# Kernel tuning notes

Hardware: AMD Instinct MI355X
Metric: run time of the kernel (lower is better)

Reference implementation:

```python
import jax, jax.numpy as jnp
import numpy as np

EPS = 1e-8


def _mp_match(v1, v2, w):
    """Fused multi-perspective cosine match.
    v1, v2: (G, L, D); w: (P, D). Returns (G, L, P).
    cos_p(l) = <w_p*v1_l, w_p*v2_l> / max(||w_p*v1_l|| * ||w_p*v2_l||, eps)
    """
    w2 = w * w  # (P, D)
    num = jnp.einsum('gld,pd->glp', v1 * v2, w2)
    n1 = jnp.sqrt(jnp.einsum('gld,pd->glp', v1 * v1, w2))
    n2 = jnp.sqrt(jnp.einsum('gld,pd->glp', v2 * v2, w2))
    return num / jnp.maximum(n1 * n2, EPS)


def setup_inputs() -> dict:
    key = jax.random.key(0)
    k1, k2 = jax.random.split(key)
    n_graphs = 64
    nodes_per_graph = 2048
    dim = 128  # must equal perspectives (mp_w is square)
    N = n_graphs * nodes_per_graph
    feats = jax.random.normal(k1, (N, dim), dtype=jnp.float32)
    graph_idx = jnp.repeat(jnp.arange(n_graphs, dtype=jnp.int64), nodes_per_graph)
    mp_w = jax.random.uniform(k2, (dim, dim), dtype=jnp.float32)  # torch.rand
    return {"feats": feats, "mp_w": mp_w, "graph_idx": graph_idx, "n_graphs": n_graphs}


def reference(feats, mp_w, graph_idx, n_graphs):
    N, d = feats.shape
    L = N // n_graphs  # equal-size graphs, graph_idx is sorted/contiguous
    g = feats.reshape(n_graphs, L, d)
    p = g[0::2]  # (G/2, L, d) premise graphs
    h = g[1::2]  # (G/2, L, d) hypothesis graphs
    # cosine_attention is a plain dot product (no normalization in source)
    att = jnp.einsum('gld,gmd->glm', p, h)        # (G/2, Lp, Lh)
    att_p = jnp.einsum('glm,gmd->gld', att, h)     # (G/2, Lp, d)
    att_h = jnp.einsum('glm,gld->gmd', att, p)     # (G/2, Lh, d)
    multi_p = _mp_match(p, att_p, mp_w)            # (G/2, Lp, P)
    multi_h = _mp_match(h, att_h, mp_w)            # (G/2, Lh, P)
    # original concatenates [p0, h0, p1, h1, ...] along node axis
    P = mp_w.shape[0]
    out = jnp.stack([multi_p, multi_h], axis=1).reshape(n_graphs * L, P)
    return out
```

## Files before the change

### kernel.cpp

```cpp
#include <hip/hip_runtime.h>
#include <math.h>

#define D 128
#define GRAPHS 64

typedef __attribute__((ext_vector_type(8))) short bf16x8;
typedef __attribute__((ext_vector_type(4))) float f32x4;

__device__ __forceinline__ unsigned short f2bf(float f) {
  union { float f; unsigned u; } v; v.f = f;
  unsigned r = v.u + 0x7fffu + ((v.u >> 16) & 1u);
  return (unsigned short)(r >> 16);
}
__device__ __forceinline__ float bf2f(unsigned short h) {
  union { unsigned u; float f; } v; v.u = ((unsigned)h) << 16;
  return v.f;
}
__device__ __forceinline__ unsigned short truncbf(float f) {
  union { float f; unsigned u; } v; v.f = f;
  return (unsigned short)(v.u >> 16);
}

__global__ __launch_bounds__(256) void gram_mfma_kernel(
    const float* __restrict__ feats, float* __restrict__ partial,
    int L, int KS) {
  const int g = blockIdx.x / KS;
  const int s = blockIdx.x - g * KS;
  const int chunk = L / KS;
  const float* __restrict__ X = feats + ((size_t)g * L + (size_t)s * chunk) * D;

  __shared__ unsigned short sXT[128][40];
  const int tid = threadIdx.x;
  const int wv = tid >> 6, lane = tid & 63, quad = lane >> 4, ln = lane & 15;

  f32x4 acc[2][8];
#pragma unroll
  for (int rt = 0; rt < 2; ++rt)
#pragma unroll
    for (int ct = 0; ct < 8; ++ct) acc[rt][ct] = (f32x4)(0.f);

  for (int k0 = 0; k0 < chunk; k0 += 32) {
    __syncthreads();
#pragma unroll
    for (int v = 0; v < 2; ++v) {
      int idx = tid + v * 256;
      int k2 = idx & 15, d4 = idx >> 4;
      int k = k2 * 2, dd = d4 * 4;
      float4 r0 = *(const float4*)(X + (size_t)(k0 + k) * D + dd);
      float4 r1 = *(const float4*)(X + (size_t)(k0 + k + 1) * D + dd);
      const float* p0 = (const float*)&r0;
      const float* p1 = (const float*)&r1;
#pragma unroll
      for (int i = 0; i < 4; ++i) {
        unsigned pack = (unsigned)f2bf(p0[i]) | ((unsigned)f2bf(p1[i]) << 16);
        *(unsigned*)&sXT[dd + i][k] = pack;
      }
    }
    __syncthreads();
    bf16x8 af[2], bfr[8];
#pragma unroll
    for (int rt = 0; rt < 2; ++rt)
      af[rt] = *(const bf16x8*)&sXT[32 * wv + 16 * rt + ln][quad * 8];
#pragma unroll
    for (int ct = 0; ct < 8; ++ct)
      bfr[ct] = *(const bf16x8*)&sXT[16 * ct + ln][quad * 8];
#pragma unroll
    for (int rt = 0; rt < 2; ++rt)
#pragma unroll
      for (int ct = 0; ct < 8; ++ct)
        acc[rt][ct] = __builtin_amdgcn_mfma_f32_16x16x32_bf16(
            af[rt], bfr[ct], acc[rt][ct], 0, 0, 0);
  }

  float* P = partial + (size_t)blockIdx.x * (D * D);
#pragma unroll
  for (int rt = 0; rt < 2; ++rt)
#pragma unroll
    for (int ct = 0; ct < 8; ++ct)
#pragma unroll
      for (int r = 0; r < 4; ++r)
        P[(size_t)(32 * wv + 16 * rt + quad * 4 + r) * D + 16 * ct + ln] =
            acc[rt][ct][r];
}

__global__ __launch_bounds__(256) void gram_reduce_bf_kernel(
    const float* __restrict__ partial, unsigned short* __restrict__ gram,
    int KS) {
  int idx = blockIdx.x * 256 + threadIdx.x;
  int g = idx >> 14;
  const float* P = partial + (size_t)g * KS * (D * D) + (idx & (D * D - 1));
  float s = 0.f;
  for (int k = 0; k < KS; ++k) s += P[(size_t)k * (D * D)];
  gram[idx] = f2bf(s);
}

__global__ __launch_bounds__(256) void w2_kernel(
    const float* __restrict__ w, unsigned short* __restrict__ w2) {
  int idx = blockIdx.x * 256 + threadIdx.x;
  float v = w[idx];
  w2[idx] = f2bf(v * v);
}

__global__ __launch_bounds__(256) void fused_mfma_kernel(
    const float* __restrict__ feats, const unsigned short* __restrict__ gram,
    const unsigned short* __restrict__ w2, float* __restrict__ out, int L) {
  const int tiles = L / 32;
  const int gi = blockIdx.x / tiles;
  const int row0 = (blockIdx.x - gi * tiles) * 32;
  const float* __restrict__ A = feats + ((size_t)gi * L + row0) * D;
  const unsigned short* __restrict__ G = gram + (size_t)(gi ^ 1) * (D * D);
  float* __restrict__ O = out + ((size_t)gi * L + row0) * D;

  __shared__ unsigned short sA[32][136];
  __shared__ unsigned short sV[32][136];
  __shared__ unsigned short sB[128][136];

  const int tid = threadIdx.x;
  const int wv = tid >> 6, lane = tid & 63, quad = lane >> 4, ln = lane & 15;

#pragma unroll
  for (int v = 0; v < 4; ++v) {
    int idx = tid + v * 256;
    int r = idx >> 5, c4 = idx & 31;
    float4 t = *(const float4*)(A + (size_t)r * D + c4 * 4);
    unsigned lo = (unsigned)f2bf(t.x) | ((unsigned)f2bf(t.y) << 16);
    unsigned hi = (unsigned)f2bf(t.z) | ((unsigned)f2bf(t.w) << 16);
    *(unsigned*)&sA[r][c4 * 4] = lo;
    *(unsigned*)&sA[r][c4 * 4 + 2] = hi;
  }
#pragma unroll
  for (int v = 0; v < 8; ++v) {
    int idx = tid + v * 256;
    int r = idx >> 4, c16 = idx & 15;
    uint4 t = *(const uint4*)(G + (size_t)r * D + c16 * 8);
    *(uint4*)&sB[r][c16 * 8] = t;
  }
  __syncthreads();

  f32x4 acc[2][2];
#pragma unroll
  for (int rt = 0; rt < 2; ++rt)
#pragma unroll
    for (int ct = 0; ct < 2; ++ct) acc[rt][ct] = (f32x4)(0.f);

#pragma unroll
  for (int kc = 0; kc < 4; ++kc) {
    bf16x8 af[2], bfr[2];
#pragma unroll
    for (int rt = 0; rt < 2; ++rt)
      af[rt] = *(const bf16x8*)&sA[16 * rt + ln][kc * 32 + quad * 8];
#pragma unroll
    for (int ct = 0; ct < 2; ++ct)
      bfr[ct] = *(const bf16x8*)&sB[32 * wv + 16 * ct + ln][kc * 32 + quad * 8];
#pragma unroll
    for (int rt = 0; rt < 2; ++rt)
#pragma unroll
      for (int ct = 0; ct < 2; ++ct)
        acc[rt][ct] = __builtin_amdgcn_mfma_f32_16x16x32_bf16(
            af[rt], bfr[ct], acc[rt][ct], 0, 0, 0);
  }
#pragma unroll
  for (int rt = 0; rt < 2; ++rt)
#pragma unroll
    for (int ct = 0; ct < 2; ++ct)
#pragma unroll
      for (int r = 0; r < 4; ++r)
        sV[16 * rt + quad * 4 + r][32 * wv + 16 * ct + ln] = f2bf(acc[rt][ct][r]);
  __syncthreads();

#pragma unroll
  for (int v = 0; v < 8; ++v) {
    int idx = tid + v * 256;
    int r = idx >> 4, c16 = idx & 15;
    uint4 t = *(const uint4*)(w2 + (size_t)r * D + c16 * 8);
    *(uint4*)&sB[r][c16 * 8] = t;
  }
  __syncthreads();

  f32x4 an[2][2], s1[2][2], s2[2][2];
#pragma unroll
  for (int rt = 0; rt < 2; ++rt)
#pragma unroll
    for (int ct = 0; ct < 2; ++ct) {
      an[rt][ct] = (f32x4)(0.f);
      s1[rt][ct] = (f32x4)(0.f);
      s2[rt][ct] = (f32x4)(0.f);
    }

#pragma unroll
  for (int dc = 0; dc < 4; ++dc) {
    bf16x8 fx2[2], faa[2], fvv[2];
#pragma unroll
    for (int rt = 0; rt < 2; ++rt) {
      bf16x8 xa = *(const bf16x8*)&sA[16 * rt + ln][dc * 32 + quad * 8];
      bf16x8 xv = *(const bf16x8*)&sV[16 * rt + ln][dc * 32 + quad * 8];
#pragma unroll
      for (int j = 0; j < 8; ++j) {
        float a = bf2f((unsigned short)xa[j]);
        float vv = bf2f((unsigned short)xv[j]);
        fx2[rt][j] = (short)truncbf(a * vv);
        faa[rt][j] = (short)truncbf(a * a);
        fvv[rt][j] = (short)truncbf(vv * vv);
      }
    }
    bf16x8 wf[2];
#pragma unroll
    for (int ct = 0; ct < 2; ++ct)
      wf[ct] = *(const bf16x8*)&sB[32 * wv + 16 * ct + ln][dc * 32 + quad * 8];
#pragma unroll
    for (int rt = 0; rt < 2; ++rt)
#pragma unroll
      for (int ct = 0; ct < 2; ++ct) {
        an[rt][ct] = __builtin_amdgcn_mfma_f32_16x16x32_bf16(
            fx2[rt], wf[ct], an[rt][ct], 0, 0, 0);
        s1[rt][ct] = __builtin_amdgcn_mfma_f32_16x16x32_bf16(
            faa[rt], wf[ct], s1[rt][ct], 0, 0, 0);
        s2[rt][ct] = __builtin_amdgcn_mfma_f32_16x16x32_bf16(
            fvv[rt], wf[ct], s2[rt][ct], 0, 0, 0);
      }
  }

#pragma unroll
  for (int rt = 0; rt < 2; ++rt)
#pragma unroll
    for (int ct = 0; ct < 2; ++ct)
#pragma unroll
      for (int r = 0; r < 4; ++r) {
        float num = an[rt][ct][r];
        float den = fmaxf(sqrtf(s1[rt][ct][r] * s2[rt][ct][r]), 1e-8f);
        O[(size_t)(16 * rt + quad * 4 + r) * D + 32 * wv + 16 * ct + ln] =
            num / den;
      }
}

extern "C" void kernel_launch(void* const* d_in, const int* in_sizes, int n_in,
                              void* d_out, int out_size, void* d_ws, size_t ws_size,
                              hipStream_t stream) {
  const float* feats = (const float*)d_in[0];
  const float* w = (const float*)d_in[1];
  float* out = (float*)d_out;
  const int L = (in_sizes[0] / D) / GRAPHS;

  const size_t gramF32 = (size_t)GRAPHS * D * D * sizeof(float);
  const size_t gramBF = (size_t)GRAPHS * D * D * sizeof(unsigned short);
  const size_t w2BF = (size_t)D * D * sizeof(unsigned short);
  int KS = 8;
  while (KS > 1 && (size_t)KS * gramF32 + gramBF + w2BF > ws_size) KS >>= 1;

  float* partial = (float*)d_ws;
  unsigned short* gramBuf = (unsigned short*)((char*)d_ws + (size_t)KS * gramF32);
  unsigned short* w2Buf = gramBuf + (size_t)GRAPHS * D * D;

  hipLaunchKernelGGL(w2_kernel, dim3(D * D / 256), dim3(256), 0, stream, w, w2Buf);
  hipLaunchKernelGGL(gram_mfma_kernel, dim3(GRAPHS * KS), dim3(256), 0, stream,
                     feats, partial, L, KS);
  hipLaunchKernelGGL(gram_reduce_bf_kernel, dim3(GRAPHS * D * D / 256), dim3(256),
                     0, stream, partial, gramBuf, KS);
  hipLaunchKernelGGL(fused_mfma_kernel, dim3(GRAPHS * (L / 32)), dim3(256), 0,
                     stream, feats, gramBuf, w2Buf, out, L);
}
```

Before: 166.6 us.

## Fuse gram split-K reduction into one kernel and use MFMA-fragment LDS layouts

Replaces the split-K gram kernel plus a separate global reduction pass with a single 1024-thread block per graph. Four wave groups each cover a quarter of the rows and reduce through LDS atomics before writing bf16. Both kernels now store LDS data in MFMA-fragment order so each lane reads one contiguous 16-byte vector without padding. The elementwise products use bit masks and perm packing, and the final normalisation uses rsq instead of sqrt plus divide. The risks are only 64 blocks for the gram stage (low occupancy), LDS atomic contention, and slightly changed epsilon semantics.

```diff
diff --git a/kernel.cpp b/kernel.cpp
--- a/kernel.cpp
+++ b/kernel.cpp
@@ -6,32 +6,35 @@
 
 typedef __attribute__((ext_vector_type(8))) short bf16x8;
 typedef __attribute__((ext_vector_type(4))) float f32x4;
+
+union U4H8 { uint4 u; bf16x8 h; };
 
 __device__ __forceinline__ unsigned short f2bf(float f) {
   union { float f; unsigned u; } v; v.f = f;
   unsigned r = v.u + 0x7fffu + ((v.u >> 16) & 1u);
   return (unsigned short)(r >> 16);
 }
-__device__ __forceinline__ float bf2f(unsigned short h) {
-  union { unsigned u; float f; } v; v.u = ((unsigned)h) << 16;
-  return v.f;
-}
-__device__ __forceinline__ unsigned short truncbf(float f) {
-  union { float f; unsigned u; } v; v.f = f;
-  return (unsigned short)(v.u >> 16);
-}
-
-__global__ __launch_bounds__(256) void gram_mfma_kernel(
-    const float* __restrict__ feats, float* __restrict__ partial,
-    int L, int KS) {
-  const int g = blockIdx.x / KS;
-  const int s = blockIdx.x - g * KS;
-  const int chunk = L / KS;
-  const float* __restrict__ X = feats + ((size_t)g * L + (size_t)s * chunk) * D;
-
-  __shared__ unsigned short sXT[128][40];
+__device__ __forceinline__ unsigned asu(float f) {
+  union { float f; unsigned u; } v; v.f = f; return v.u;
+}
+__device__ __forceinline__ float asf(unsigned u) {
+  union { unsigned u; float f; } v; v.u = u; return v.f;
+}
+
+__global__ __launch_bounds__(1024) void gram_kernel(
+    const float* __restrict__ feats, unsigned short* __restrict__ gram, int L) {
+  const int g = blockIdx.x;
+  const float* __restrict__ X = feats + (size_t)g * L * D;
+
+  __shared__ __align__(16) unsigned char smem[32768];
+  unsigned short* sXf = (unsigned short*)smem;
+  float* sR = (float*)smem;
+
   const int tid = threadIdx.x;
-  const int wv = tid >> 6, lane = tid & 63, quad = lane >> 4, ln = lane & 15;
+  const int wv = tid >> 6, lane = tid & 63;
+  const int kg = wv >> 2, wg = wv & 3;
+  const int quad = lane >> 4, ln = lane & 15;
+  const int tgrp = tid & 255;
 
   f32x4 acc[2][8];
 #pragma unroll
@@ -39,59 +42,68 @@
 #pragma unroll
     for (int ct = 0; ct < 8; ++ct) acc[rt][ct] = (f32x4)(0.f);
 
-  for (int k0 = 0; k0 < chunk; k0 += 32) {
+  const int Lq = L >> 2;
+  for (int it = 0; it < Lq; it += 32) {
+    const int k0 = kg * Lq + it;
     __syncthreads();
 #pragma unroll
     for (int v = 0; v < 2; ++v) {
-      int idx = tid + v * 256;
+      int idx = tgrp + v * 256;
       int k2 = idx & 15, d4 = idx >> 4;
       int k = k2 * 2, dd = d4 * 4;
       float4 r0 = *(const float4*)(X + (size_t)(k0 + k) * D + dd);
       float4 r1 = *(const float4*)(X + (size_t)(k0 + k + 1) * D + dd);
       const float* p0 = (const float*)&r0;
       const float* p1 = (const float*)&r1;
+      int qs = k >> 3, j = k & 7;
 #pragma unroll
       for (int i = 0; i < 4; ++i) {
+        int d = dd + i;
+        int t = d >> 4, lnw = d & 15;
         unsigned pack = (unsigned)f2bf(p0[i]) | ((unsigned)f2bf(p1[i]) << 16);
-        *(unsigned*)&sXT[dd + i][k] = pack;
-      }
-    }
-    __syncthreads();
-    bf16x8 af[2], bfr[8];
-#pragma unroll
-    for (int rt = 0; rt < 2; ++rt)
-      af[rt] = *(const bf16x8*)&sXT[32 * wv + 16 * rt + ln][quad * 8];
+        *(unsigned*)&sXf[((kg * 8 + t) * 64 + qs * 16 + lnw) * 8 + j] = pack;
+      }
+    }
+    __syncthreads();
+    bf16x8 bfr[8];
 #pragma unroll
     for (int ct = 0; ct < 8; ++ct)
-      bfr[ct] = *(const bf16x8*)&sXT[16 * ct + ln][quad * 8];
+      bfr[ct] = *(const bf16x8*)&sXf[((kg * 8 + ct) * 64 + lane) * 8];
 #pragma unroll
     for (int rt = 0; rt < 2; ++rt)
 #pragma unroll
       for (int ct = 0; ct < 8; ++ct)
         acc[rt][ct] = __builtin_amdgcn_mfma_f32_16x16x32_bf16(
-            af[rt], bfr[ct], acc[rt][ct], 0, 0, 0);
-  }
-
-  float* P = partial + (size_t)blockIdx.x * (D * D);
-#pragma unroll
-  for (int rt = 0; rt < 2; ++rt)
-#pragma unroll
-    for (int ct = 0; ct < 8; ++ct)
-#pragma unroll
-      for (int r = 0; r < 4; ++r)
-        P[(size_t)(32 * wv + 16 * rt + quad * 4 + r) * D + 16 * ct + ln] =
-            acc[rt][ct][r];
-}
-
-__global__ __launch_bounds__(256) void gram_reduce_bf_kernel(
-    const float* __restrict__ partial, unsigned short* __restrict__ gram,
-    int KS) {
-  int idx = blockIdx.x * 256 + threadIdx.x;
-  int g = idx >> 14;
-  const float* P = partial + (size_t)g * KS * (D * D) + (idx & (D * D - 1));
-  float s = 0.f;
-  for (int k = 0; k < KS; ++k) s += P[(size_t)k * (D * D)];
-  gram[idx] = f2bf(s);
+            bfr[2 * wg + rt], bfr[ct], acc[rt][ct], 0, 0, 0);
+  }
+
+  for (int p = 0; p < 2; ++p) {
+    __syncthreads();
+    *(float4*)&sR[tid * 8] = make_float4(0.f, 0.f, 0.f, 0.f);
+    *(float4*)&sR[tid * 8 + 4] = make_float4(0.f, 0.f, 0.f, 0.f);
+    __syncthreads();
+    if ((wg >> 1) == p) {
+#pragma unroll
+      for (int rt = 0; rt < 2; ++rt)
+#pragma unroll
+        for (int ct = 0; ct < 8; ++ct)
+#pragma unroll
+          for (int r = 0; r < 4; ++r) {
+            int row = 32 * wg + 16 * rt + quad * 4 + r;
+            atomicAdd(&sR[(row - p * 64) * 128 + 16 * ct + ln], acc[rt][ct][r]);
+          }
+    }
+    __syncthreads();
+    int rl = tid >> 4, c0 = (tid & 15) * 8;
+    float4 a = *(float4*)&sR[rl * 128 + c0];
+    float4 b = *(float4*)&sR[rl * 128 + c0 + 4];
+    uint4 o;
+    o.x = (unsigned)f2bf(a.x) | ((unsigned)f2bf(a.y) << 16);
+    o.y = (unsigned)f2bf(a.z) | ((unsigned)f2bf(a.w) << 16);
+    o.z = (unsigned)f2bf(b.x) | ((unsigned)f2bf(b.y) << 16);
+    o.w = (unsigned)f2bf(b.z) | ((unsigned)f2bf(b.w) << 16);
+    *(uint4*)&gram[(size_t)g * (D * D) + (size_t)(p * 64 + rl) * D + c0] = o;
+  }
 }
 
 __global__ __launch_bounds__(256) void w2_kernel(
@@ -101,7 +113,7 @@
   w2[idx] = f2bf(v * v);
 }
 
-__global__ __launch_bounds__(256) void fused_mfma_kernel(
+__global__ __launch_bounds__(256) void fused_kernel2(
     const float* __restrict__ feats, const unsigned short* __restrict__ gram,
     const unsigned short* __restrict__ w2, float* __restrict__ out, int L) {
   const int tiles = L / 32;
@@ -111,9 +123,9 @@
   const unsigned short* __restrict__ G = gram + (size_t)(gi ^ 1) * (D * D);
   float* __restrict__ O = out + ((size_t)gi * L + row0) * D;
 
-  __shared__ unsigned short sA[32][136];
-  __shared__ unsigned short sV[32][136];
-  __shared__ unsigned short sB[128][136];
+  __shared__ __align__(16) unsigned short sAf[4096];
+  __shared__ __align__(16) unsigned short sVf[4096];
+  __shared__ __align__(16) unsigned short sBf[16384];
 
   const int tid = threadIdx.x;
   const int wv = tid >> 6, lane = tid & 63, quad = lane >> 4, ln = lane & 15;
@@ -123,17 +135,20 @@
     int idx = tid + v * 256;
     int r = idx >> 5, c4 = idx & 31;
     float4 t = *(const float4*)(A + (size_t)r * D + c4 * 4);
-    unsigned lo = (unsigned)f2bf(t.x) | ((unsigned)f2bf(t.y) << 16);
-    unsigned hi = (unsigned)f2bf(t.z) | ((unsigned)f2bf(t.w) << 16);
-    *(unsigned*)&sA[r][c4 * 4] = lo;
-    *(unsigned*)&sA[r][c4 * 4 + 2] = hi;
+    int kc = c4 >> 3, qd = (c4 & 7) >> 1, j0 = (c4 & 1) * 4;
+    int rt = r >> 4, lnw = r & 15;
+    uint2 pk;
+    pk.x = (unsigned)f2bf(t.x) | ((unsigned)f2bf(t.y) << 16);
+    pk.y = (unsigned)f2bf(t.z) | ((unsigned)f2bf(t.w) << 16);
+    *(uint2*)&sAf[((kc * 2 + rt) * 64 + qd * 16 + lnw) * 8 + j0] = pk;
   }
 #pragma unroll
   for (int v = 0; v < 8; ++v) {
     int idx = tid + v * 256;
     int r = idx >> 4, c16 = idx & 15;
     uint4 t = *(const uint4*)(G + (size_t)r * D + c16 * 8);
-    *(uint4*)&sB[r][c16 * 8] = t;
+    int kc = c16 >> 2, qd = c16 & 3, tb = r >> 4, lnw = r & 15;
+    *(uint4*)&sBf[((kc * 8 + tb) * 64 + qd * 16 + lnw) * 8] = t;
   }
   __syncthreads();
 
@@ -142,16 +157,15 @@
   for (int rt = 0; rt < 2; ++rt)
 #pragma unroll
     for (int ct = 0; ct < 2; ++ct) acc[rt][ct] = (f32x4)(0.f);
-
 #pragma unroll
   for (int kc = 0; kc < 4; ++kc) {
     bf16x8 af[2], bfr[2];
 #pragma unroll
     for (int rt = 0; rt < 2; ++rt)
-      af[rt] = *(const bf16x8*)&sA[16 * rt + ln][kc * 32 + quad * 8];
-#pragma unroll
-    for (int ct = 0; ct < 2; ++ct)
-      bfr[ct] = *(const bf16x8*)&sB[32 * wv + 16 * ct + ln][kc * 32 + quad * 8];
+      af[rt] = *(const bf16x8*)&sAf[((kc * 2 + rt) * 64 + lane) * 8];
+#pragma unroll
+    for (int ct = 0; ct < 2; ++ct)
+      bfr[ct] = *(const bf16x8*)&sBf[((kc * 8 + 2 * wv + ct) * 64 + lane) * 8];
 #pragma unroll
     for (int rt = 0; rt < 2; ++rt)
 #pragma unroll
@@ -165,7 +179,8 @@
     for (int ct = 0; ct < 2; ++ct)
 #pragma unroll
       for (int r = 0; r < 4; ++r)
-        sV[16 * rt + quad * 4 + r][32 * wv + 16 * ct + ln] = f2bf(acc[rt][ct][r]);
+        sVf[((wv * 2 + rt) * 64 + (2 * ct + (ln >> 3)) * 16 + quad * 4 + r) * 8 +
+            (ln & 7)] = f2bf(acc[rt][ct][r]);
   __syncthreads();
 
 #pragma unroll
@@ -173,7 +188,8 @@
     int idx = tid + v * 256;
     int r = idx >> 4, c16 = idx & 15;
     uint4 t = *(const uint4*)(w2 + (size_t)r * D + c16 * 8);
-    *(uint4*)&sB[r][c16 * 8] = t;
+    int kc = c16 >> 2, qd = c16 & 3, tb = r >> 4, lnw = r & 15;
+    *(uint4*)&sBf[((kc * 8 + tb) * 64 + qd * 16 + lnw) * 8] = t;
   }
   __syncthreads();
 
@@ -186,37 +202,41 @@
       s1[rt][ct] = (f32x4)(0.f);
       s2[rt][ct] = (f32x4)(0.f);
     }
-
 #pragma unroll
   for (int dc = 0; dc < 4; ++dc) {
-    bf16x8 fx2[2], faa[2], fvv[2];
+    U4H8 fx2[2], faa[2], fvv[2];
 #pragma unroll
     for (int rt = 0; rt < 2; ++rt) {
-      bf16x8 xa = *(const bf16x8*)&sA[16 * rt + ln][dc * 32 + quad * 8];
-      bf16x8 xv = *(const bf16x8*)&sV[16 * rt + ln][dc * 32 + quad * 8];
-#pragma unroll
-      for (int j = 0; j < 8; ++j) {
-        float a = bf2f((unsigned short)xa[j]);
-        float vv = bf2f((unsigned short)xv[j]);
-        fx2[rt][j] = (short)truncbf(a * vv);
-        faa[rt][j] = (short)truncbf(a * a);
-        fvv[rt][j] = (short)truncbf(vv * vv);
+      uint4 ua = *(const uint4*)&sAf[((dc * 2 + rt) * 64 + lane) * 8];
+      uint4 uv = *(const uint4*)&sVf[((dc * 2 + rt) * 64 + lane) * 8];
+      const unsigned* uap = &ua.x;
+      const unsigned* uvp = &uv.x;
+#pragma unroll
+      for (int w = 0; w < 4; ++w) {
+        float a0 = asf(uap[w] << 16), a1 = asf(uap[w] & 0xFFFF0000u);
+        float v0 = asf(uvp[w] << 16), v1 = asf(uvp[w] & 0xFFFF0000u);
+        (&fx2[rt].u.x)[w] =
+            __builtin_amdgcn_perm(asu(a1 * v1), asu(a0 * v0), 0x07060302u);
+        (&faa[rt].u.x)[w] =
+            __builtin_amdgcn_perm(asu(a1 * a1), asu(a0 * a0), 0x07060302u);
+        (&fvv[rt].u.x)[w] =
+            __builtin_amdgcn_perm(asu(v1 * v1), asu(v0 * v0), 0x07060302u);
       }
     }
     bf16x8 wf[2];
 #pragma unroll
     for (int ct = 0; ct < 2; ++ct)
-      wf[ct] = *(const bf16x8*)&sB[32 * wv + 16 * ct + ln][dc * 32 + quad * 8];
+      wf[ct] = *(const bf16x8*)&sBf[((dc * 8 + 2 * wv + ct) * 64 + lane) * 8];
 #pragma unroll
     for (int rt = 0; rt < 2; ++rt)
 #pragma unroll
       for (int ct = 0; ct < 2; ++ct) {
         an[rt][ct] = __builtin_amdgcn_mfma_f32_16x16x32_bf16(
-            fx2[rt], wf[ct], an[rt][ct], 0, 0, 0);
+            fx2[rt].h, wf[ct], an[rt][ct], 0, 0, 0);
         s1[rt][ct] = __builtin_amdgcn_mfma_f32_16x16x32_bf16(
-            faa[rt], wf[ct], s1[rt][ct], 0, 0, 0);
+            faa[rt].h, wf[ct], s1[rt][ct], 0, 0, 0);
         s2[rt][ct] = __builtin_amdgcn_mfma_f32_16x16x32_bf16(
-            fvv[rt], wf[ct], s2[rt][ct], 0, 0, 0);
+            fvv[rt].h, wf[ct], s2[rt][ct], 0, 0, 0);
       }
   }
 
@@ -226,10 +246,9 @@
     for (int ct = 0; ct < 2; ++ct)
 #pragma unroll
       for (int r = 0; r < 4; ++r) {
-        float num = an[rt][ct][r];
-        float den = fmaxf(sqrtf(s1[rt][ct][r] * s2[rt][ct][r]), 1e-8f);
+        float t = fmaxf(s1[rt][ct][r] * s2[rt][ct][r], 1e-16f);
         O[(size_t)(16 * rt + quad * 4 + r) * D + 32 * wv + 16 * ct + ln] =
-            num / den;
+            an[rt][ct][r] * __builtin_amdgcn_rsqf(t);
       }
 }
 
@@ -241,21 +260,12 @@
   float* out = (float*)d_out;
   const int L = (in_sizes[0] / D) / GRAPHS;
 
-  const size_t gramF32 = (size_t)GRAPHS * D * D * sizeof(float);
-  const size_t gramBF = (size_t)GRAPHS * D * D * sizeof(unsigned short);
-  const size_t w2BF = (size_t)D * D * sizeof(unsigned short);
-  int KS = 8;
-  while (KS > 1 && (size_t)KS * gramF32 + gramBF + w2BF > ws_size) KS >>= 1;
-
-  float* partial = (float*)d_ws;
-  unsigned short* gramBuf = (unsigned short*)((char*)d_ws + (size_t)KS * gramF32);
+  unsigned short* gramBuf = (unsigned short*)d_ws;
   unsigned short* w2Buf = gramBuf + (size_t)GRAPHS * D * D;
 
   hipLaunchKernelGGL(w2_kernel, dim3(D * D / 256), dim3(256), 0, stream, w, w2Buf);
-  hipLaunchKernelGGL(gram_mfma_kernel, dim3(GRAPHS * KS), dim3(256), 0, stream,
-                     feats, partial, L, KS);
-  hipLaunchKernelGGL(gram_reduce_bf_kernel, dim3(GRAPHS * D * D / 256), dim3(256),
-                     0, stream, partial, gramBuf, KS);
-  hipLaunchKernelGGL(fused_mfma_kernel, dim3(GRAPHS * (L / 32)), dim3(256), 0,
+  hipLaunchKernelGGL(gram_kernel, dim3(GRAPHS), dim3(1024), 0, stream,
+                     feats, gramBuf, L);
+  hipLaunchKernelGGL(fused_kernel2, dim3(GRAPHS * (L / 32)), dim3(256), 0,
                      stream, feats, gramBuf, w2Buf, out, L);
 }
```

Result: slower. 344.2 us (+106.6%).
